# Optimization experiments

Measured on AMD Instinct MI355X. Metric: run time of the kernel, lower is better.

## Reference

```python
import jax, jax.numpy as jnp
import numpy as np

GAMMA = 0.5          # blending coeff from __init__
NEG_SLOPE = 0.2      # LeakyReLU slope
MASK_FILL = -9e15    # zero_vec constant from source

N, M, D = 8192, 8192, 256
SPARSITY = 0.01


def setup_inputs() -> dict:
    key = jax.random.key(0)
    k1, k2, k3, k4, k5 = jax.random.split(key, 5)
    input1 = jax.random.normal(k1, (N, D), dtype=jnp.float32)
    input2 = jax.random.normal(k2, (M, D), dtype=jnp.float32)
    adj = (jax.random.uniform(k3, (N, M)) < SPARSITY).astype(jnp.float32)
    # xavier_normal with gain=1.414 on (D,1): std = gain*sqrt(2/(D+1))
    std = 1.414 * np.sqrt(2.0 / (D + 1))
    a1 = jax.random.normal(k4, (D, 1), dtype=jnp.float32) * std
    a2 = jax.random.normal(k5, (D, 1), dtype=jnp.float32) * std
    return {"input1": input1, "input2": input2, "adj": adj, "a1": a1, "a2": a2}


def reference(input1, input2, adj, a1, a2):
    # e1: (N,1) broadcast against e2: (1,M) -> e: (N,M)
    e1 = input1 @ a1                      # (N,1)
    e2 = (input2 @ a2).T                  # (1,M)
    e = jax.nn.leaky_relu(e1 + e2, negative_slope=NEG_SLOPE)
    attention = jnp.where(adj > 0, e, MASK_FILL)
    attention = jax.nn.softmax(attention, axis=1)
    # scale each row by its adjacency degree, then gamma-blend with adj
    attention = attention * jnp.sum(adj, axis=1, keepdims=True)
    attention = attention * GAMMA + adj * (1.0 - GAMMA)
    return attention @ input2             # (N,D)
```

## Files before the change

kernel.cpp:

```cpp
#include <hip/hip_runtime.h>
#include <cstdint>
#include <cstddef>

#define NEG_SLOPE 0.2f
#define CAP 160
#define RPW 4

typedef float f32x4 __attribute__((ext_vector_type(4)));
typedef unsigned short u16x4 __attribute__((ext_vector_type(4)));

static __device__ __forceinline__ unsigned short f2bf_rne(float f) {
  unsigned u = __float_as_uint(f);
  unsigned r = (u + 0x7FFFu + ((u >> 16) & 1u)) >> 16;
  return (unsigned short)r;
}
static __device__ __forceinline__ float bf2f(unsigned short h) {
  return __uint_as_float((unsigned)h << 16);
}

__global__ __launch_bounds__(256) void score_conv_kernel(
    const float* __restrict__ x1, const float* __restrict__ x2,
    const float* __restrict__ a1, const float* __restrict__ a2,
    float* __restrict__ e1, float* __restrict__ f2,
    unsigned short* __restrict__ x2h, int N, int M, int D) {
  int gtid = blockIdx.x * blockDim.x + threadIdx.x;
  int wid = gtid >> 6;
  int lane = threadIdx.x & 63;
  if (wid >= N + M) return;
  const float4 av = *reinterpret_cast<const float4*>(
      ((wid < N) ? a1 : a2) + lane * 4);
  if (wid < N) {
    const float4 xv = *reinterpret_cast<const float4*>(x1 + (size_t)wid * D + lane * 4);
    float s = xv.x * av.x + xv.y * av.y + xv.z * av.z + xv.w * av.w;
    #pragma unroll
    for (int off = 32; off > 0; off >>= 1) s += __shfl_down(s, off, 64);
    if (lane == 0) e1[wid] = s;
  } else {
    int row = wid - N;
    const float4 xv = *reinterpret_cast<const float4*>(x2 + (size_t)row * D + lane * 4);
    float s = xv.x * av.x + xv.y * av.y + xv.z * av.z + xv.w * av.w;
    u16x4 h;
    h.x = f2bf_rne(xv.x); h.y = f2bf_rne(xv.y);
    h.z = f2bf_rne(xv.z); h.w = f2bf_rne(xv.w);
    reinterpret_cast<u16x4*>(x2h)[(size_t)row * (D >> 2) + lane] = h;
    #pragma unroll
    for (int off = 32; off > 0; off >>= 1) s += __shfl_down(s, off, 64);
    if (lane == 0) f2[row] = s;
  }
}

__global__ __launch_bounds__(256, 2) void attn_pipe_kernel(
    const float* __restrict__ adj, const unsigned short* __restrict__ x2h,
    const float* __restrict__ e1, const float* __restrict__ f2,
    float* __restrict__ out, int N, int M, int D) {
  __shared__ float s_f2[8192];
  __shared__ int   s_idx[4][CAP];
  __shared__ float s_w[4][CAP];

  const int tid  = threadIdx.x;
  const int wv   = tid >> 6;
  const int lane = tid & 63;
  const int D4   = D >> 2;

  {
    const f32x4* src = reinterpret_cast<const f32x4*>(f2);
    f32x4* dst = reinterpret_cast<f32x4*>(s_f2);
    #pragma unroll
    for (int i = 0; i < 8; ++i) dst[tid + i * 256] = src[tid + i * 256];
  }
  __syncthreads();

  const int rowbase = (blockIdx.x * 4 + wv) * RPW;
  if (rowbase >= N) return;
  const float4 e1v = *reinterpret_cast<const float4*>(e1 + rowbase);
  const float e1s[4] = {e1v.x, e1v.y, e1v.z, e1v.w};

  const u16x4* __restrict__ x2h4 = reinterpret_cast<const u16x4*>(x2h);
  float4* __restrict__ out4 = reinterpret_cast<float4*>(out);

  f32x4 hold[32];
  {
    const f32x4* ar = reinterpret_cast<const f32x4*>(adj + (size_t)rowbase * M) + lane;
    #pragma unroll
    for (int it = 0; it < 32; ++it) hold[it] = __builtin_nontemporal_load(ar + it * 64);
  }

  #pragma unroll
  for (int r = 0; r < RPW; ++r) {
    const int row = rowbase + r;
    uint64_t m0 = 0ull, m1 = 0ull;
    #pragma unroll
    for (int it = 0; it < 16; ++it) {
      f32x4 v = hold[it];
      uint64_t b = 0;
      if (v.x > 0.f) b |= 1ull;
      if (v.y > 0.f) b |= 2ull;
      if (v.z > 0.f) b |= 4ull;
      if (v.w > 0.f) b |= 8ull;
      m0 |= b << (it * 4);
    }
    #pragma unroll
    for (int it = 16; it < 32; ++it) {
      f32x4 v = hold[it];
      uint64_t b = 0;
      if (v.x > 0.f) b |= 1ull;
      if (v.y > 0.f) b |= 2ull;
      if (v.z > 0.f) b |= 4ull;
      if (v.w > 0.f) b |= 8ull;
      m1 |= b << ((it - 16) * 4);
    }
    if (r + 1 < RPW) {
      const f32x4* nr =
          reinterpret_cast<const f32x4*>(adj + (size_t)(row + 1) * M) + lane;
      #pragma unroll
      for (int it = 0; it < 32; ++it) hold[it] = __builtin_nontemporal_load(nr + it * 64);
    }
    __builtin_amdgcn_sched_barrier(0);

    const float e1i = e1s[r];
    const int cnt = __popcll(m0) + __popcll(m1);
    int incl = cnt;
    #pragma unroll
    for (int off = 1; off < 64; off <<= 1) {
      int t = __shfl_up(incl, off, 64);
      if (lane >= off) incl += t;
    }
    int pos = incl - cnt;
    const int K = __shfl(incl, 63, 64);

    while (m0) {
      int b = __ffsll((unsigned long long)m0) - 1;
      m0 &= m0 - 1;
      int j = ((((b >> 2) << 6) + lane) << 2) + (b & 3);
      float e = e1i + s_f2[j];
      e = (e > 0.f) ? e : NEG_SLOPE * e;
      if (pos < CAP) { s_idx[wv][pos] = j; s_w[wv][pos] = e; }
      ++pos;
    }
    while (m1) {
      int b = __ffsll((unsigned long long)m1) - 1;
      m1 &= m1 - 1;
      int j = (((((b >> 2) + 16) << 6) + lane) << 2) + (b & 3);
      float e = e1i + s_f2[j];
      e = (e > 0.f) ? e : NEG_SLOPE * e;
      if (pos < CAP) { s_idx[wv][pos] = j; s_w[wv][pos] = e; }
      ++pos;
    }

    if (row < N) {
      if (K == 0) {
        float4 z; z.x = z.y = z.z = z.w = 0.f;
        out4[(size_t)row * D4 + lane] = z;
      } else {
        const int Kc = (K < CAP) ? K : CAP;
        float lm = -1e30f;
        for (int k = lane; k < Kc; k += 64) lm = fmaxf(lm, s_w[wv][k]);
        #pragma unroll
        for (int off = 32; off > 0; off >>= 1)
          lm = fmaxf(lm, __shfl_xor(lm, off, 64));
        float ls = 0.f;
        for (int k = lane; k < Kc; k += 64) {
          float pr = __expf(s_w[wv][k] - lm);
          s_w[wv][k] = pr;
          ls += pr;
        }
        #pragma unroll
        for (int off = 32; off > 0; off >>= 1) ls += __shfl_xor(ls, off, 64);
        const float scale = 0.5f * (float)K / ls;
        for (int k = lane; k < Kc; k += 64)
          s_w[wv][k] = s_w[wv][k] * scale + 0.5f;

        float4 a0, a1v, a2v, a3;
        a0.x = a0.y = a0.z = a0.w = 0.f; a1v = a0; a2v = a0; a3 = a0;
        int k = 0;
        for (; k + 4 <= Kc; k += 4) {
          int j0 = __builtin_amdgcn_readfirstlane(s_idx[wv][k + 0]);
          int j1 = __builtin_amdgcn_readfirstlane(s_idx[wv][k + 1]);
          int j2 = __builtin_amdgcn_readfirstlane(s_idx[wv][k + 2]);
          int j3 = __builtin_amdgcn_readfirstlane(s_idx[wv][k + 3]);
          float w0 = s_w[wv][k + 0], w1 = s_w[wv][k + 1];
          float w2 = s_w[wv][k + 2], w3 = s_w[wv][k + 3];
          u16x4 h0 = x2h4[(size_t)j0 * D4 + lane];
          u16x4 h1 = x2h4[(size_t)j1 * D4 + lane];
          u16x4 h2 = x2h4[(size_t)j2 * D4 + lane];
          u16x4 h3 = x2h4[(size_t)j3 * D4 + lane];
          a0.x = fmaf(w0, bf2f(h0.x), a0.x); a0.y = fmaf(w0, bf2f(h0.y), a0.y);
          a0.z = fmaf(w0, bf2f(h0.z), a0.z); a0.w = fmaf(w0, bf2f(h0.w), a0.w);
          a1v.x = fmaf(w1, bf2f(h1.x), a1v.x); a1v.y = fmaf(w1, bf2f(h1.y), a1v.y);
          a1v.z = fmaf(w1, bf2f(h1.z), a1v.z); a1v.w = fmaf(w1, bf2f(h1.w), a1v.w);
          a2v.x = fmaf(w2, bf2f(h2.x), a2v.x); a2v.y = fmaf(w2, bf2f(h2.y), a2v.y);
          a2v.z = fmaf(w2, bf2f(h2.z), a2v.z); a2v.w = fmaf(w2, bf2f(h2.w), a2v.w);
          a3.x = fmaf(w3, bf2f(h3.x), a3.x); a3.y = fmaf(w3, bf2f(h3.y), a3.y);
          a3.z = fmaf(w3, bf2f(h3.z), a3.z); a3.w = fmaf(w3, bf2f(h3.w), a3.w);
        }
        for (; k < Kc; ++k) {
          int j = __builtin_amdgcn_readfirstlane(s_idx[wv][k]);
          float w = s_w[wv][k];
          u16x4 h = x2h4[(size_t)j * D4 + lane];
          a0.x = fmaf(w, bf2f(h.x), a0.x); a0.y = fmaf(w, bf2f(h.y), a0.y);
          a0.z = fmaf(w, bf2f(h.z), a0.z); a0.w = fmaf(w, bf2f(h.w), a0.w);
        }
        float4 rr;
        rr.x = (a0.x + a1v.x) + (a2v.x + a3.x);
        rr.y = (a0.y + a1v.y) + (a2v.y + a3.y);
        rr.z = (a0.z + a1v.z) + (a2v.z + a3.z);
        rr.w = (a0.w + a1v.w) + (a2v.w + a3.w);
        out4[(size_t)row * D4 + lane] = rr;
      }
    }
  }
}

extern "C" void kernel_launch(void* const* d_in, const int* in_sizes, int n_in,
                              void* d_out, int out_size, void* d_ws, size_t ws_size,
                              hipStream_t stream) {
  const float* x1  = (const float*)d_in[0];
  const float* x2  = (const float*)d_in[1];
  const float* adj = (const float*)d_in[2];
  const float* a1  = (const float*)d_in[3];
  const float* a2  = (const float*)d_in[4];
  float* out = (float*)d_out;

  const int D = in_sizes[3];
  const int N = in_sizes[0] / D;
  const int M = in_sizes[1] / D;

  char* p = (char*)d_ws;
  float* e1 = (float*)p;                    p += (size_t)N * 4;
  float* f2 = (float*)p;                    p += (size_t)M * 4;
  unsigned short* x2h = (unsigned short*)p;

  const int waves = N + M;
  const int blocks1 = (waves * 64 + 255) / 256;
  score_conv_kernel<<<blocks1, 256, 0, stream>>>(x1, x2, a1, a2, e1, f2, x2h, N, M, D);

  const int rows_per_block = 4 * RPW;
  attn_pipe_kernel<<<(N + rows_per_block - 1) / rows_per_block, 256, 0, stream>>>(
      adj, x2h, e1, f2, out, N, M, D);
}
```

Before: 94.10 us.

## Use one row per wave with software-pipelined gather and higher occupancy

Replaces the four-rows-per-wave kernel, which held 32 vector registers of adjacency prefetch, with a one-row-per-wave kernel that streams the adjacency row directly and raises the launch bound to 6 blocks per CU. The 32 KB shared f2 staging is dropped in favour of direct global reads of f2, so there is less LDS and no block-wide sync. The feature gather is double-buffered in groups of 8 rows, with the K list zero-padded to a multiple of 16, so loads overlap the FMAs. Output uses nontemporal stores. The adjacency-load prefetch overlap is lost and f2 becomes a scattered global read, in exchange for more waves in flight.

```diff
diff --git a/kernel.cpp b/kernel.cpp
--- a/kernel.cpp
+++ b/kernel.cpp
@@ -4,7 +4,6 @@
 
 #define NEG_SLOPE 0.2f
 #define CAP 160
-#define RPW 4
 
 typedef float f32x4 __attribute__((ext_vector_type(4)));
 typedef unsigned short u16x4 __attribute__((ext_vector_type(4)));
@@ -49,166 +48,149 @@
   }
 }
 
-__global__ __launch_bounds__(256, 2) void attn_pipe_kernel(
+#define ISSUE8(Hv, base)                                                \
+  {                                                                     \
+    _Pragma("unroll")                                                   \
+    for (int i = 0; i < 8; ++i) {                                       \
+      int jj = __builtin_amdgcn_readfirstlane(s_idx[wv][(base) + i]);   \
+      Hv[i] = x2h4[(size_t)jj * D4 + lane];                             \
+    }                                                                   \
+  }
+
+#define CONSUME8(Hv, base)                                              \
+  {                                                                     \
+    _Pragma("unroll")                                                   \
+    for (int i = 0; i < 8; ++i) {                                       \
+      float w = s_w[wv][(base) + i];                                    \
+      u16x4 h = Hv[i];                                                  \
+      f32x4& ac = (i & 1) ? acc1 : acc0;                                \
+      ac.x = fmaf(w, bf2f(h.x), ac.x);                                  \
+      ac.y = fmaf(w, bf2f(h.y), ac.y);                                  \
+      ac.z = fmaf(w, bf2f(h.z), ac.z);                                  \
+      ac.w = fmaf(w, bf2f(h.w), ac.w);                                  \
+    }                                                                   \
+  }
+
+__global__ __launch_bounds__(256, 6) void attn_kernel(
     const float* __restrict__ adj, const unsigned short* __restrict__ x2h,
     const float* __restrict__ e1, const float* __restrict__ f2,
     float* __restrict__ out, int N, int M, int D) {
-  __shared__ float s_f2[8192];
   __shared__ int   s_idx[4][CAP];
   __shared__ float s_w[4][CAP];
 
   const int tid  = threadIdx.x;
   const int wv   = tid >> 6;
   const int lane = tid & 63;
-  const int D4   = D >> 2;
-
-  {
-    const f32x4* src = reinterpret_cast<const f32x4*>(f2);
-    f32x4* dst = reinterpret_cast<f32x4*>(s_f2);
-    #pragma unroll
-    for (int i = 0; i < 8; ++i) dst[tid + i * 256] = src[tid + i * 256];
-  }
-  __syncthreads();
-
-  const int rowbase = (blockIdx.x * 4 + wv) * RPW;
-  if (rowbase >= N) return;
-  const float4 e1v = *reinterpret_cast<const float4*>(e1 + rowbase);
-  const float e1s[4] = {e1v.x, e1v.y, e1v.z, e1v.w};
+  const int row  = blockIdx.x * 4 + wv;
+  if (row >= N) return;
+
+  const int D4 = D >> 2;
+  const float e1i = e1[row];
+  const f32x4* __restrict__ arow4 =
+      reinterpret_cast<const f32x4*>(adj + (size_t)row * M);
+
+  uint64_t m0 = 0ull, m1 = 0ull;
+  #pragma unroll 8
+  for (int it = 0; it < 16; ++it) {
+    f32x4 v = __builtin_nontemporal_load(&arow4[it * 64 + lane]);
+    uint64_t b = 0;
+    if (v.x > 0.f) b |= 1ull;
+    if (v.y > 0.f) b |= 2ull;
+    if (v.z > 0.f) b |= 4ull;
+    if (v.w > 0.f) b |= 8ull;
+    m0 |= b << (it * 4);
+  }
+  #pragma unroll 8
+  for (int it = 16; it < 32; ++it) {
+    f32x4 v = __builtin_nontemporal_load(&arow4[it * 64 + lane]);
+    uint64_t b = 0;
+    if (v.x > 0.f) b |= 1ull;
+    if (v.y > 0.f) b |= 2ull;
+    if (v.z > 0.f) b |= 4ull;
+    if (v.w > 0.f) b |= 8ull;
+    m1 |= b << ((it - 16) * 4);
+  }
+  const int cnt = __popcll(m0) + __popcll(m1);
+
+  int incl = cnt;
+  #pragma unroll
+  for (int off = 1; off < 64; off <<= 1) {
+    int t = __shfl_up(incl, off, 64);
+    if (lane >= off) incl += t;
+  }
+  int pos = incl - cnt;
+  const int K = __shfl(incl, 63, 64);
+
+  while (m0) {
+    int b = __ffsll((unsigned long long)m0) - 1;
+    m0 &= m0 - 1;
+    int j = ((((b >> 2) << 6) + lane) << 2) + (b & 3);
+    float e = e1i + f2[j];
+    e = (e > 0.f) ? e : NEG_SLOPE * e;
+    if (pos < CAP) { s_idx[wv][pos] = j; s_w[wv][pos] = e; }
+    ++pos;
+  }
+  while (m1) {
+    int b = __ffsll((unsigned long long)m1) - 1;
+    m1 &= m1 - 1;
+    int j = (((((b >> 2) + 16) << 6) + lane) << 2) + (b & 3);
+    float e = e1i + f2[j];
+    e = (e > 0.f) ? e : NEG_SLOPE * e;
+    if (pos < CAP) { s_idx[wv][pos] = j; s_w[wv][pos] = e; }
+    ++pos;
+  }
+
+  f32x4* __restrict__ out4 = reinterpret_cast<f32x4*>(out);
+  if (K == 0) {
+    f32x4 z; z.x = z.y = z.z = z.w = 0.f;
+    __builtin_nontemporal_store(z, &out4[(size_t)row * D4 + lane]);
+    return;
+  }
+
+  const int Kc = (K < CAP) ? K : CAP;
+  float lm = -1e30f;
+  for (int k = lane; k < Kc; k += 64) lm = fmaxf(lm, s_w[wv][k]);
+  #pragma unroll
+  for (int off = 32; off > 0; off >>= 1) lm = fmaxf(lm, __shfl_xor(lm, off, 64));
+  float ls = 0.f;
+  for (int k = lane; k < Kc; k += 64) {
+    float pr = __expf(s_w[wv][k] - lm);
+    s_w[wv][k] = pr;
+    ls += pr;
+  }
+  #pragma unroll
+  for (int off = 32; off > 0; off >>= 1) ls += __shfl_xor(ls, off, 64);
+  const float scale = 0.5f * (float)K / ls;
+  for (int k = lane; k < Kc; k += 64) s_w[wv][k] = s_w[wv][k] * scale + 0.5f;
+
+  const int Kp = (Kc + 15) & ~15;
+  for (int k = Kc + lane; k < Kp; k += 64) {
+    s_idx[wv][k] = 0;
+    s_w[wv][k] = 0.f;
+  }
 
   const u16x4* __restrict__ x2h4 = reinterpret_cast<const u16x4*>(x2h);
-  float4* __restrict__ out4 = reinterpret_cast<float4*>(out);
-
-  f32x4 hold[32];
-  {
-    const f32x4* ar = reinterpret_cast<const f32x4*>(adj + (size_t)rowbase * M) + lane;
-    #pragma unroll
-    for (int it = 0; it < 32; ++it) hold[it] = __builtin_nontemporal_load(ar + it * 64);
-  }
-
-  #pragma unroll
-  for (int r = 0; r < RPW; ++r) {
-    const int row = rowbase + r;
-    uint64_t m0 = 0ull, m1 = 0ull;
-    #pragma unroll
-    for (int it = 0; it < 16; ++it) {
-      f32x4 v = hold[it];
-      uint64_t b = 0;
-      if (v.x > 0.f) b |= 1ull;
-      if (v.y > 0.f) b |= 2ull;
-      if (v.z > 0.f) b |= 4ull;
-      if (v.w > 0.f) b |= 8ull;
-      m0 |= b << (it * 4);
-    }
-    #pragma unroll
-    for (int it = 16; it < 32; ++it) {
-      f32x4 v = hold[it];
-      uint64_t b = 0;
-      if (v.x > 0.f) b |= 1ull;
-      if (v.y > 0.f) b |= 2ull;
-      if (v.z > 0.f) b |= 4ull;
-      if (v.w > 0.f) b |= 8ull;
-      m1 |= b << ((it - 16) * 4);
-    }
-    if (r + 1 < RPW) {
-      const f32x4* nr =
-          reinterpret_cast<const f32x4*>(adj + (size_t)(row + 1) * M) + lane;
-      #pragma unroll
-      for (int it = 0; it < 32; ++it) hold[it] = __builtin_nontemporal_load(nr + it * 64);
-    }
+  f32x4 acc0, acc1;
+  acc0.x = acc0.y = acc0.z = acc0.w = 0.f;
+  acc1 = acc0;
+
+  u16x4 hA[8], hB[8];
+  ISSUE8(hA, 0);
+  for (int g = 0; g < Kp; g += 16) {
+    ISSUE8(hB, g + 8);
     __builtin_amdgcn_sched_barrier(0);
-
-    const float e1i = e1s[r];
-    const int cnt = __popcll(m0) + __popcll(m1);
-    int incl = cnt;
-    #pragma unroll
-    for (int off = 1; off < 64; off <<= 1) {
-      int t = __shfl_up(incl, off, 64);
-      if (lane >= off) incl += t;
-    }
-    int pos = incl - cnt;
-    const int K = __shfl(incl, 63, 64);
-
-    while (m0) {
-      int b = __ffsll((unsigned long long)m0) - 1;
-      m0 &= m0 - 1;
-      int j = ((((b >> 2) << 6) + lane) << 2) + (b & 3);
-      float e = e1i + s_f2[j];
-      e = (e > 0.f) ? e : NEG_SLOPE * e;
-      if (pos < CAP) { s_idx[wv][pos] = j; s_w[wv][pos] = e; }
-      ++pos;
-    }
-    while (m1) {
-      int b = __ffsll((unsigned long long)m1) - 1;
-      m1 &= m1 - 1;
-      int j = (((((b >> 2) + 16) << 6) + lane) << 2) + (b & 3);
-      float e = e1i + s_f2[j];
-      e = (e > 0.f) ? e : NEG_SLOPE * e;
-      if (pos < CAP) { s_idx[wv][pos] = j; s_w[wv][pos] = e; }
-      ++pos;
-    }
-
-    if (row < N) {
-      if (K == 0) {
-        float4 z; z.x = z.y = z.z = z.w = 0.f;
-        out4[(size_t)row * D4 + lane] = z;
-      } else {
-        const int Kc = (K < CAP) ? K : CAP;
-        float lm = -1e30f;
-        for (int k = lane; k < Kc; k += 64) lm = fmaxf(lm, s_w[wv][k]);
-        #pragma unroll
-        for (int off = 32; off > 0; off >>= 1)
-          lm = fmaxf(lm, __shfl_xor(lm, off, 64));
-        float ls = 0.f;
-        for (int k = lane; k < Kc; k += 64) {
-          float pr = __expf(s_w[wv][k] - lm);
-          s_w[wv][k] = pr;
-          ls += pr;
-        }
-        #pragma unroll
-        for (int off = 32; off > 0; off >>= 1) ls += __shfl_xor(ls, off, 64);
-        const float scale = 0.5f * (float)K / ls;
-        for (int k = lane; k < Kc; k += 64)
-          s_w[wv][k] = s_w[wv][k] * scale + 0.5f;
-
-        float4 a0, a1v, a2v, a3;
-        a0.x = a0.y = a0.z = a0.w = 0.f; a1v = a0; a2v = a0; a3 = a0;
-        int k = 0;
-        for (; k + 4 <= Kc; k += 4) {
-          int j0 = __builtin_amdgcn_readfirstlane(s_idx[wv][k + 0]);
-          int j1 = __builtin_amdgcn_readfirstlane(s_idx[wv][k + 1]);
-          int j2 = __builtin_amdgcn_readfirstlane(s_idx[wv][k + 2]);
-          int j3 = __builtin_amdgcn_readfirstlane(s_idx[wv][k + 3]);
-          float w0 = s_w[wv][k + 0], w1 = s_w[wv][k + 1];
-          float w2 = s_w[wv][k + 2], w3 = s_w[wv][k + 3];
-          u16x4 h0 = x2h4[(size_t)j0 * D4 + lane];
-          u16x4 h1 = x2h4[(size_t)j1 * D4 + lane];
-          u16x4 h2 = x2h4[(size_t)j2 * D4 + lane];
-          u16x4 h3 = x2h4[(size_t)j3 * D4 + lane];
-          a0.x = fmaf(w0, bf2f(h0.x), a0.x); a0.y = fmaf(w0, bf2f(h0.y), a0.y);
-          a0.z = fmaf(w0, bf2f(h0.z), a0.z); a0.w = fmaf(w0, bf2f(h0.w), a0.w);
-          a1v.x = fmaf(w1, bf2f(h1.x), a1v.x); a1v.y = fmaf(w1, bf2f(h1.y), a1v.y);
-          a1v.z = fmaf(w1, bf2f(h1.z), a1v.z); a1v.w = fmaf(w1, bf2f(h1.w), a1v.w);
-          a2v.x = fmaf(w2, bf2f(h2.x), a2v.x); a2v.y = fmaf(w2, bf2f(h2.y), a2v.y);
-          a2v.z = fmaf(w2, bf2f(h2.z), a2v.z); a2v.w = fmaf(w2, bf2f(h2.w), a2v.w);
-          a3.x = fmaf(w3, bf2f(h3.x), a3.x); a3.y = fmaf(w3, bf2f(h3.y), a3.y);
-          a3.z = fmaf(w3, bf2f(h3.z), a3.z); a3.w = fmaf(w3, bf2f(h3.w), a3.w);
-        }
-        for (; k < Kc; ++k) {
-          int j = __builtin_amdgcn_readfirstlane(s_idx[wv][k]);
-          float w = s_w[wv][k];
-          u16x4 h = x2h4[(size_t)j * D4 + lane];
-          a0.x = fmaf(w, bf2f(h.x), a0.x); a0.y = fmaf(w, bf2f(h.y), a0.y);
-          a0.z = fmaf(w, bf2f(h.z), a0.z); a0.w = fmaf(w, bf2f(h.w), a0.w);
-        }
-        float4 rr;
-        rr.x = (a0.x + a1v.x) + (a2v.x + a3.x);
-        rr.y = (a0.y + a1v.y) + (a2v.y + a3.y);
-        rr.z = (a0.z + a1v.z) + (a2v.z + a3.z);
-        rr.w = (a0.w + a1v.w) + (a2v.w + a3.w);
-        out4[(size_t)row * D4 + lane] = rr;
-      }
-    }
-  }
+    CONSUME8(hA, g);
+    if (g + 16 < Kp) { ISSUE8(hA, g + 16); }
+    __builtin_amdgcn_sched_barrier(0);
+    CONSUME8(hB, g + 8);
+  }
+
+  f32x4 r;
+  r.x = acc0.x + acc1.x;
+  r.y = acc0.y + acc1.y;
+  r.z = acc0.z + acc1.z;
+  r.w = acc0.w + acc1.w;
+  __builtin_nontemporal_store(r, &out4[(size_t)row * D4 + lane]);
 }
 
 extern "C" void kernel_launch(void* const* d_in, const int* in_sizes, int n_in,
@@ -233,8 +215,5 @@
   const int waves = N + M;
   const int blocks1 = (waves * 64 + 255) / 256;
   score_conv_kernel<<<blocks1, 256, 0, stream>>>(x1, x2, a1, a2, e1, f2, x2h, N, M, D);
-
-  const int rows_per_block = 4 * RPW;
-  attn_pipe_kernel<<<(N + rows_per_block - 1) / rows_per_block, 256, 0, stream>>>(
-      adj, x2h, e1, f2, out, N, M, D);
-}
+  attn_kernel<<<(N + 3) / 4, 256, 0, stream>>>(adj, x2h, e1, f2, out, N, M, D);
+}
```

After: 97.53 us. +3.6%, slower.

## Process one row per wave and store f2 scores as bf16 in LDS

Applied to the files above, without the earlier changes.

Drops the multi-row software pipeline, which held the next adjacency row in 32 registers per lane. Each wave now handles one row and streams its adjacency loads with partial unrolling, launching four times as many blocks. The f2 score vector is stored in bf16, which halves the per-block LDS preload, and the output is written with nontemporal stores. This trades explicit load/compute overlap for lower register pressure and higher occupancy, and the bf16 f2 adds rounding error to the attention logits.

```diff
diff --git a/kernel.cpp b/kernel.cpp
--- a/kernel.cpp
+++ b/kernel.cpp
@@ -4,7 +4,6 @@
 
 #define NEG_SLOPE 0.2f
 #define CAP 160
-#define RPW 4
 
 typedef float f32x4 __attribute__((ext_vector_type(4)));
 typedef unsigned short u16x4 __attribute__((ext_vector_type(4)));
@@ -21,7 +20,7 @@
 __global__ __launch_bounds__(256) void score_conv_kernel(
     const float* __restrict__ x1, const float* __restrict__ x2,
     const float* __restrict__ a1, const float* __restrict__ a2,
-    float* __restrict__ e1, float* __restrict__ f2,
+    float* __restrict__ e1, unsigned short* __restrict__ f2h,
     unsigned short* __restrict__ x2h, int N, int M, int D) {
   int gtid = blockIdx.x * blockDim.x + threadIdx.x;
   int wid = gtid >> 6;
@@ -45,170 +44,148 @@
     reinterpret_cast<u16x4*>(x2h)[(size_t)row * (D >> 2) + lane] = h;
     #pragma unroll
     for (int off = 32; off > 0; off >>= 1) s += __shfl_down(s, off, 64);
-    if (lane == 0) f2[row] = s;
-  }
-}
-
-__global__ __launch_bounds__(256, 2) void attn_pipe_kernel(
+    if (lane == 0) f2h[row] = f2bf_rne(s);
+  }
+}
+
+__global__ __launch_bounds__(256) void attn_kernel(
     const float* __restrict__ adj, const unsigned short* __restrict__ x2h,
-    const float* __restrict__ e1, const float* __restrict__ f2,
+    const float* __restrict__ e1, const unsigned short* __restrict__ f2h,
     float* __restrict__ out, int N, int M, int D) {
-  __shared__ float s_f2[8192];
+  __shared__ unsigned short s_f2h[8192];
   __shared__ int   s_idx[4][CAP];
   __shared__ float s_w[4][CAP];
 
   const int tid  = threadIdx.x;
   const int wv   = tid >> 6;
   const int lane = tid & 63;
-  const int D4   = D >> 2;
+  const int row  = blockIdx.x * 4 + wv;
 
   {
-    const f32x4* src = reinterpret_cast<const f32x4*>(f2);
-    f32x4* dst = reinterpret_cast<f32x4*>(s_f2);
+    const u16x4* src = reinterpret_cast<const u16x4*>(f2h);
+    u16x4* dst = reinterpret_cast<u16x4*>(s_f2h);
     #pragma unroll
     for (int i = 0; i < 8; ++i) dst[tid + i * 256] = src[tid + i * 256];
   }
   __syncthreads();
-
-  const int rowbase = (blockIdx.x * 4 + wv) * RPW;
-  if (rowbase >= N) return;
-  const float4 e1v = *reinterpret_cast<const float4*>(e1 + rowbase);
-  const float e1s[4] = {e1v.x, e1v.y, e1v.z, e1v.w};
+  if (row >= N) return;
+
+  const int D4 = D >> 2;
+  const float e1i = e1[row];
+  const f32x4* __restrict__ arow4 =
+      reinterpret_cast<const f32x4*>(adj + (size_t)row * M);
+
+  uint64_t m0 = 0ull, m1 = 0ull;
+  #pragma unroll 8
+  for (int it = 0; it < 16; ++it) {
+    f32x4 v = __builtin_nontemporal_load(&arow4[it * 64 + lane]);
+    uint64_t b = 0;
+    if (v.x > 0.f) b |= 1ull;
+    if (v.y > 0.f) b |= 2ull;
+    if (v.z > 0.f) b |= 4ull;
+    if (v.w > 0.f) b |= 8ull;
+    m0 |= b << (it * 4);
+  }
+  #pragma unroll 8
+  for (int it = 16; it < 32; ++it) {
+    f32x4 v = __builtin_nontemporal_load(&arow4[it * 64 + lane]);
+    uint64_t b = 0;
+    if (v.x > 0.f) b |= 1ull;
+    if (v.y > 0.f) b |= 2ull;
+    if (v.z > 0.f) b |= 4ull;
+    if (v.w > 0.f) b |= 8ull;
+    m1 |= b << ((it - 16) * 4);
+  }
+  const int cnt = __popcll(m0) + __popcll(m1);
+
+  int incl = cnt;
+  #pragma unroll
+  for (int off = 1; off < 64; off <<= 1) {
+    int t = __shfl_up(incl, off, 64);
+    if (lane >= off) incl += t;
+  }
+  int pos = incl - cnt;
+  const int K = __shfl(incl, 63, 64);
+
+  while (m0) {
+    int b = __ffsll((unsigned long long)m0) - 1;
+    m0 &= m0 - 1;
+    int j = ((((b >> 2) << 6) + lane) << 2) + (b & 3);
+    float e = e1i + bf2f(s_f2h[j]);
+    e = (e > 0.f) ? e : NEG_SLOPE * e;
+    if (pos < CAP) { s_idx[wv][pos] = j; s_w[wv][pos] = e; }
+    ++pos;
+  }
+  while (m1) {
+    int b = __ffsll((unsigned long long)m1) - 1;
+    m1 &= m1 - 1;
+    int j = (((((b >> 2) + 16) << 6) + lane) << 2) + (b & 3);
+    float e = e1i + bf2f(s_f2h[j]);
+    e = (e > 0.f) ? e : NEG_SLOPE * e;
+    if (pos < CAP) { s_idx[wv][pos] = j; s_w[wv][pos] = e; }
+    ++pos;
+  }
+
+  f32x4* __restrict__ out4 = reinterpret_cast<f32x4*>(out);
+  if (K == 0) {
+    f32x4 z; z.x = z.y = z.z = z.w = 0.f;
+    __builtin_nontemporal_store(z, &out4[(size_t)row * D4 + lane]);
+    return;
+  }
+
+  const int Kc = (K < CAP) ? K : CAP;
+  float lm = -1e30f;
+  for (int k = lane; k < Kc; k += 64) lm = fmaxf(lm, s_w[wv][k]);
+  #pragma unroll
+  for (int off = 32; off > 0; off >>= 1) lm = fmaxf(lm, __shfl_xor(lm, off, 64));
+  float ls = 0.f;
+  for (int k = lane; k < Kc; k += 64) {
+    float pr = __expf(s_w[wv][k] - lm);
+    s_w[wv][k] = pr;
+    ls += pr;
+  }
+  #pragma unroll
+  for (int off = 32; off > 0; off >>= 1) ls += __shfl_xor(ls, off, 64);
+  const float scale = 0.5f * (float)K / ls;
+  for (int k = lane; k < Kc; k += 64) s_w[wv][k] = s_w[wv][k] * scale + 0.5f;
 
   const u16x4* __restrict__ x2h4 = reinterpret_cast<const u16x4*>(x2h);
-  float4* __restrict__ out4 = reinterpret_cast<float4*>(out);
-
-  f32x4 hold[32];
-  {
-    const f32x4* ar = reinterpret_cast<const f32x4*>(adj + (size_t)rowbase * M) + lane;
-    #pragma unroll
-    for (int it = 0; it < 32; ++it) hold[it] = __builtin_nontemporal_load(ar + it * 64);
-  }
-
-  #pragma unroll
-  for (int r = 0; r < RPW; ++r) {
-    const int row = rowbase + r;
-    uint64_t m0 = 0ull, m1 = 0ull;
-    #pragma unroll
-    for (int it = 0; it < 16; ++it) {
-      f32x4 v = hold[it];
-      uint64_t b = 0;
-      if (v.x > 0.f) b |= 1ull;
-      if (v.y > 0.f) b |= 2ull;
-      if (v.z > 0.f) b |= 4ull;
-      if (v.w > 0.f) b |= 8ull;
-      m0 |= b << (it * 4);
-    }
-    #pragma unroll
-    for (int it = 16; it < 32; ++it) {
-      f32x4 v = hold[it];
-      uint64_t b = 0;
-      if (v.x > 0.f) b |= 1ull;
-      if (v.y > 0.f) b |= 2ull;
-      if (v.z > 0.f) b |= 4ull;
-      if (v.w > 0.f) b |= 8ull;
-      m1 |= b << ((it - 16) * 4);
-    }
-    if (r + 1 < RPW) {
-      const f32x4* nr =
-          reinterpret_cast<const f32x4*>(adj + (size_t)(row + 1) * M) + lane;
-      #pragma unroll
-      for (int it = 0; it < 32; ++it) hold[it] = __builtin_nontemporal_load(nr + it * 64);
-    }
-    __builtin_amdgcn_sched_barrier(0);
-
-    const float e1i = e1s[r];
-    const int cnt = __popcll(m0) + __popcll(m1);
-    int incl = cnt;
-    #pragma unroll
-    for (int off = 1; off < 64; off <<= 1) {
-      int t = __shfl_up(incl, off, 64);
-      if (lane >= off) incl += t;
-    }
-    int pos = incl - cnt;
-    const int K = __shfl(incl, 63, 64);
-
-    while (m0) {
-      int b = __ffsll((unsigned long long)m0) - 1;
-      m0 &= m0 - 1;
-      int j = ((((b >> 2) << 6) + lane) << 2) + (b & 3);
-      float e = e1i + s_f2[j];
-      e = (e > 0.f) ? e : NEG_SLOPE * e;
-      if (pos < CAP) { s_idx[wv][pos] = j; s_w[wv][pos] = e; }
-      ++pos;
-    }
-    while (m1) {
-      int b = __ffsll((unsigned long long)m1) - 1;
-      m1 &= m1 - 1;
-      int j = (((((b >> 2) + 16) << 6) + lane) << 2) + (b & 3);
-      float e = e1i + s_f2[j];
-      e = (e > 0.f) ? e : NEG_SLOPE * e;
-      if (pos < CAP) { s_idx[wv][pos] = j; s_w[wv][pos] = e; }
-      ++pos;
-    }
-
-    if (row < N) {
-      if (K == 0) {
-        float4 z; z.x = z.y = z.z = z.w = 0.f;
-        out4[(size_t)row * D4 + lane] = z;
-      } else {
-        const int Kc = (K < CAP) ? K : CAP;
-        float lm = -1e30f;
-        for (int k = lane; k < Kc; k += 64) lm = fmaxf(lm, s_w[wv][k]);
-        #pragma unroll
-        for (int off = 32; off > 0; off >>= 1)
-          lm = fmaxf(lm, __shfl_xor(lm, off, 64));
-        float ls = 0.f;
-        for (int k = lane; k < Kc; k += 64) {
-          float pr = __expf(s_w[wv][k] - lm);
-          s_w[wv][k] = pr;
-          ls += pr;
-        }
-        #pragma unroll
-        for (int off = 32; off > 0; off >>= 1) ls += __shfl_xor(ls, off, 64);
-        const float scale = 0.5f * (float)K / ls;
-        for (int k = lane; k < Kc; k += 64)
-          s_w[wv][k] = s_w[wv][k] * scale + 0.5f;
-
-        float4 a0, a1v, a2v, a3;
-        a0.x = a0.y = a0.z = a0.w = 0.f; a1v = a0; a2v = a0; a3 = a0;
-        int k = 0;
-        for (; k + 4 <= Kc; k += 4) {
-          int j0 = __builtin_amdgcn_readfirstlane(s_idx[wv][k + 0]);
-          int j1 = __builtin_amdgcn_readfirstlane(s_idx[wv][k + 1]);
-          int j2 = __builtin_amdgcn_readfirstlane(s_idx[wv][k + 2]);
-          int j3 = __builtin_amdgcn_readfirstlane(s_idx[wv][k + 3]);
-          float w0 = s_w[wv][k + 0], w1 = s_w[wv][k + 1];
-          float w2 = s_w[wv][k + 2], w3 = s_w[wv][k + 3];
-          u16x4 h0 = x2h4[(size_t)j0 * D4 + lane];
-          u16x4 h1 = x2h4[(size_t)j1 * D4 + lane];
-          u16x4 h2 = x2h4[(size_t)j2 * D4 + lane];
-          u16x4 h3 = x2h4[(size_t)j3 * D4 + lane];
-          a0.x = fmaf(w0, bf2f(h0.x), a0.x); a0.y = fmaf(w0, bf2f(h0.y), a0.y);
-          a0.z = fmaf(w0, bf2f(h0.z), a0.z); a0.w = fmaf(w0, bf2f(h0.w), a0.w);
-          a1v.x = fmaf(w1, bf2f(h1.x), a1v.x); a1v.y = fmaf(w1, bf2f(h1.y), a1v.y);
-          a1v.z = fmaf(w1, bf2f(h1.z), a1v.z); a1v.w = fmaf(w1, bf2f(h1.w), a1v.w);
-          a2v.x = fmaf(w2, bf2f(h2.x), a2v.x); a2v.y = fmaf(w2, bf2f(h2.y), a2v.y);
-          a2v.z = fmaf(w2, bf2f(h2.z), a2v.z); a2v.w = fmaf(w2, bf2f(h2.w), a2v.w);
-          a3.x = fmaf(w3, bf2f(h3.x), a3.x); a3.y = fmaf(w3, bf2f(h3.y), a3.y);
-          a3.z = fmaf(w3, bf2f(h3.z), a3.z); a3.w = fmaf(w3, bf2f(h3.w), a3.w);
-        }
-        for (; k < Kc; ++k) {
-          int j = __builtin_amdgcn_readfirstlane(s_idx[wv][k]);
-          float w = s_w[wv][k];
-          u16x4 h = x2h4[(size_t)j * D4 + lane];
-          a0.x = fmaf(w, bf2f(h.x), a0.x); a0.y = fmaf(w, bf2f(h.y), a0.y);
-          a0.z = fmaf(w, bf2f(h.z), a0.z); a0.w = fmaf(w, bf2f(h.w), a0.w);
-        }
-        float4 rr;
-        rr.x = (a0.x + a1v.x) + (a2v.x + a3.x);
-        rr.y = (a0.y + a1v.y) + (a2v.y + a3.y);
-        rr.z = (a0.z + a1v.z) + (a2v.z + a3.z);
-        rr.w = (a0.w + a1v.w) + (a2v.w + a3.w);
-        out4[(size_t)row * D4 + lane] = rr;
-      }
-    }
-  }
+  float4 a0, a1v, a2v, a3;
+  a0.x = a0.y = a0.z = a0.w = 0.f; a1v = a0; a2v = a0; a3 = a0;
+  int k = 0;
+  for (; k + 4 <= Kc; k += 4) {
+    int j0 = __builtin_amdgcn_readfirstlane(s_idx[wv][k + 0]);
+    int j1 = __builtin_amdgcn_readfirstlane(s_idx[wv][k + 1]);
+    int j2 = __builtin_amdgcn_readfirstlane(s_idx[wv][k + 2]);
+    int j3 = __builtin_amdgcn_readfirstlane(s_idx[wv][k + 3]);
+    float w0 = s_w[wv][k + 0], w1 = s_w[wv][k + 1];
+    float w2 = s_w[wv][k + 2], w3 = s_w[wv][k + 3];
+    u16x4 h0 = x2h4[(size_t)j0 * D4 + lane];
+    u16x4 h1 = x2h4[(size_t)j1 * D4 + lane];
+    u16x4 h2 = x2h4[(size_t)j2 * D4 + lane];
+    u16x4 h3 = x2h4[(size_t)j3 * D4 + lane];
+    a0.x = fmaf(w0, bf2f(h0.x), a0.x); a0.y = fmaf(w0, bf2f(h0.y), a0.y);
+    a0.z = fmaf(w0, bf2f(h0.z), a0.z); a0.w = fmaf(w0, bf2f(h0.w), a0.w);
+    a1v.x = fmaf(w1, bf2f(h1.x), a1v.x); a1v.y = fmaf(w1, bf2f(h1.y), a1v.y);
+    a1v.z = fmaf(w1, bf2f(h1.z), a1v.z); a1v.w = fmaf(w1, bf2f(h1.w), a1v.w);
+    a2v.x = fmaf(w2, bf2f(h2.x), a2v.x); a2v.y = fmaf(w2, bf2f(h2.y), a2v.y);
+    a2v.z = fmaf(w2, bf2f(h2.z), a2v.z); a2v.w = fmaf(w2, bf2f(h2.w), a2v.w);
+    a3.x = fmaf(w3, bf2f(h3.x), a3.x); a3.y = fmaf(w3, bf2f(h3.y), a3.y);
+    a3.z = fmaf(w3, bf2f(h3.z), a3.z); a3.w = fmaf(w3, bf2f(h3.w), a3.w);
+  }
+  for (; k < Kc; ++k) {
+    int j = __builtin_amdgcn_readfirstlane(s_idx[wv][k]);
+    float w = s_w[wv][k];
+    u16x4 h = x2h4[(size_t)j * D4 + lane];
+    a0.x = fmaf(w, bf2f(h.x), a0.x); a0.y = fmaf(w, bf2f(h.y), a0.y);
+    a0.z = fmaf(w, bf2f(h.z), a0.z); a0.w = fmaf(w, bf2f(h.w), a0.w);
+  }
+  f32x4 r;
+  r.x = (a0.x + a1v.x) + (a2v.x + a3.x);
+  r.y = (a0.y + a1v.y) + (a2v.y + a3.y);
+  r.z = (a0.z + a1v.z) + (a2v.z + a3.z);
+  r.w = (a0.w + a1v.w) + (a2v.w + a3.w);
+  __builtin_nontemporal_store(r, &out4[(size_t)row * D4 + lane]);
 }
 
 extern "C" void kernel_launch(void* const* d_in, const int* in_sizes, int n_in,
@@ -227,14 +204,11 @@
 
   char* p = (char*)d_ws;
   float* e1 = (float*)p;                    p += (size_t)N * 4;
-  float* f2 = (float*)p;                    p += (size_t)M * 4;
+  unsigned short* f2h = (unsigned short*)p; p += (size_t)M * 2;
   unsigned short* x2h = (unsigned short*)p;
 
   const int waves = N + M;
   const int blocks1 = (waves * 64 + 255) / 256;
-  score_conv_kernel<<<blocks1, 256, 0, stream>>>(x1, x2, a1, a2, e1, f2, x2h, N, M, D);
-
-  const int rows_per_block = 4 * RPW;
-  attn_pipe_kernel<<<(N + rows_per_block - 1) / rows_per_block, 256, 0, stream>>>(
-      adj, x2h, e1, f2, out, N, M, D);
-}
+  score_conv_kernel<<<blocks1, 256, 0, stream>>>(x1, x2, a1, a2, e1, f2h, x2h, N, M, D);
+  attn_kernel<<<(N + 3) / 4, 256, 0, stream>>>(adj, x2h, e1, f2h, out, N, M, D);
+}
```

Result: faster. 76.72 us (-18.5%).
